# Performance work log

Measured on AMD Instinct MI355X. Metric: run time of the kernel, lower is better.

## Reference

```python
import jax, jax.numpy as jnp
import numpy as np
from jax import lax

N = 1024          # n_ligand == n_receptor == feature dim (required by broadcast in source)
D = 1024          # gnn_input_dim == gnn_output_dim
H = 32            # hopi_output_dim
C = 32            # cnn_channels


def setup_inputs() -> dict:
    key = jax.random.key(0)
    ks = jax.random.split(key, 24)
    s = 0.02
    inp = {
        "ligand_node_features": jax.random.normal(ks[0], (N, D), jnp.float32),
        "ligand_edge_features": jax.random.normal(ks[1], (N, D), jnp.float32),
        "ligand_adjacency": jax.random.uniform(ks[2], (N, N), jnp.float32),
        "receptor_node_features": jax.random.normal(ks[3], (N, D), jnp.float32),
        "receptor_edge_features": jax.random.normal(ks[4], (N, D), jnp.float32),
        "receptor_adjacency": jax.random.uniform(ks[5], (N, N), jnp.float32),
        # GNNLayer params (shared between ligand and receptor, as in source)
        "Wn": jax.random.normal(ks[6], (D, D), jnp.float32) * s,
        "bn": jax.random.normal(ks[7], (D,), jnp.float32) * s,
        "We": jax.random.normal(ks[8], (D, D), jnp.float32) * s,
        "be": jax.random.normal(ks[9], (D,), jnp.float32) * s,
        "Wa": jax.random.normal(ks[10], (1, D), jnp.float32) * s,
        "ba": jax.random.normal(ks[11], (1,), jnp.float32) * s,
        # HighOrderPairwiseInteraction: Linear(2*D -> H)
        "W_hopi": jax.random.normal(ks[12], (H, 2 * D), jnp.float32) * s,
        "b_hopi": jax.random.normal(ks[13], (H,), jnp.float32) * s,
        # CNN tail
        "conv1_w": jax.random.normal(ks[14], (C, H, 3, 3), jnp.float32) * s,
        "conv1_b": jax.random.normal(ks[15], (C,), jnp.float32) * s,
        "conv2_w": jax.random.normal(ks[16], (C, C, 3, 3), jnp.float32) * s,
        "conv2_b": jax.random.normal(ks[17], (C,), jnp.float32) * s,
        "conv3_w": jax.random.normal(ks[18], (1, C, 1, 1), jnp.float32) * s,
        "conv3_b": jax.random.normal(ks[19], (1,), jnp.float32) * s,
    }
    return inp


def _gnn(nf, ef, Wn, bn, We, be, Wa, ba):
    # aggregated: [N, D]
    agg = jnp.tanh(nf @ Wn.T + bn + ef @ We.T + be)
    scores = agg @ Wa.T + ba                      # [N, 1]
    attn = jax.nn.softmax(scores, axis=1)         # softmax over size-1 dim -> ones (faithful)
    weighted = jnp.sum(agg * attn, axis=1)        # [N]
    return nf + weighted                          # [N,D] + [N] broadcasts over last dim (D == N)


def _conv(x, w, b):
    y = lax.conv_general_dilated(x, w, (1, 1), "SAME",
                                 dimension_numbers=("NCHW", "OIHW", "NCHW"))
    return y + b[None, :, None, None]


def reference(ligand_node_features, ligand_edge_features, ligand_adjacency,
              receptor_node_features, receptor_edge_features, receptor_adjacency,
              Wn, bn, We, be, Wa, ba, W_hopi, b_hopi,
              conv1_w, conv1_b, conv2_w, conv2_b, conv3_w, conv3_b):
    lig = _gnn(ligand_node_features, ligand_edge_features, Wn, bn, We, be, Wa, ba)
    rec = _gnn(receptor_node_features, receptor_edge_features, Wn, bn, We, be, Wa, ba)

    # HOPI: interactions[i, j] = Linear(cat(lig[i], rec[j])) == lig[i] @ Wl.T + rec[j] @ Wr.T + b
    Wl, Wr = W_hopi[:, :D], W_hopi[:, D:]
    lig_p = lig @ Wl.T                            # [N, H]
    rec_p = rec @ Wr.T                            # [N, H]
    interactions = lig_p[:, None, :] + rec_p[None, :, :] + b_hopi  # [N, N, H]

    x = jnp.transpose(interactions, (2, 0, 1))[None]  # [1, H, N, N]
    x = jax.nn.relu(_conv(x, conv1_w, conv1_b))
    x = jax.nn.relu(_conv(x, conv2_w, conv2_b))
    x = _conv(x, conv3_w, conv3_b)                # [1, 1, N, N]
    return x[0, 0]                                # [N, N]
```

## Files before the change

### kernel.cpp

```cpp
#include <hip/hip_runtime.h>


typedef _Float16 half8 __attribute__((ext_vector_type(8)));
typedef _Float16 half4 __attribute__((ext_vector_type(4)));
typedef float    f32x4 __attribute__((ext_vector_type(4)));

__device__ __forceinline__ short f2h_bits(float f){
    _Float16 h = (_Float16)f;
    return __builtin_bit_cast(short, h);
}
__device__ __forceinline__ half8 pack2(const float4& x, const float4& y){
    half8 r;
    r[0] = (_Float16)x.x; r[1] = (_Float16)x.y;
    r[2] = (_Float16)x.z; r[3] = (_Float16)x.w;
    r[4] = (_Float16)y.x; r[5] = (_Float16)y.y;
    r[6] = (_Float16)y.z; r[7] = (_Float16)y.w;
    return r;
}
__device__ __forceinline__ float tanh_fast(float x){
    float e = __expf(2.f * x);
    return 1.f - 2.f / (e + 1.f);
}

#define SWZ(c) ((((c) >> 1) & 3) << 3)

__global__ __launch_bounds__(512) void gnn_kernel(
    const float* __restrict__ lig_nf, const float* __restrict__ lig_ef,
    const float* __restrict__ rec_nf, const float* __restrict__ rec_ef,
    const float* __restrict__ Wn, const float* __restrict__ We,
    const float* __restrict__ bn, const float* __restrict__ be,
    float* __restrict__ part)
{
    __shared__ __attribute__((aligned(16))) short As[128 * 64];
    __shared__ __attribute__((aligned(16))) short Bs[64 * 64];
    __shared__ float red[128][2];

    const int t  = threadIdx.x;
    const int cx = blockIdx.z;
    const float* A0 = cx ? rec_nf : lig_nf;
    const float* A1 = cx ? rec_ef : lig_ef;
    const int j0 = blockIdx.x * 128;
    const int d0 = blockIdx.y * 64;

    const int wid  = t >> 6;
    const int wm   = wid >> 1;
    const int wn   = wid & 1;
    const int lane = t & 63;
    const int lr   = lane & 15;
    const int lg   = lane >> 4;

    f32x4 acc[2][2];
    #pragma unroll
    for (int m = 0; m < 2; ++m)
        #pragma unroll
        for (int n = 0; n < 2; ++n)
            acc[m][n] = (f32x4){0.f, 0.f, 0.f, 0.f};

    const int arow = t >> 2;
    const int akc  = (t & 3) * 16;
    const int brow = t >> 3;
    const int bkc  = (t & 7) * 8;

    float4 av[4], bv[2];
    {
        const float* ap = A0 + (size_t)(j0 + arow) * 1024 + akc;
        const float* bp = Wn + (size_t)(d0 + brow) * 1024 + bkc;
        #pragma unroll
        for (int q = 0; q < 4; ++q) av[q] = *reinterpret_cast<const float4*>(ap + q * 4);
        #pragma unroll
        for (int q = 0; q < 2; ++q) bv[q] = *reinterpret_cast<const float4*>(bp + q * 4);
    }

    for (int kb = 0; kb < 2048; kb += 64){
        __syncthreads();
        {
            const int ga = (t & 3) * 2;
            const int sa = arow & 7;
            *reinterpret_cast<half8*>(&As[arow * 64 + ((ga    ) ^ sa) * 8]) = pack2(av[0], av[1]);
            *reinterpret_cast<half8*>(&As[arow * 64 + ((ga + 1) ^ sa) * 8]) = pack2(av[2], av[3]);
            *reinterpret_cast<half8*>(&Bs[brow * 64 + (((t & 7)) ^ (brow & 7)) * 8]) = pack2(bv[0], bv[1]);
        }
        {
            const int kbn = (kb + 64) & 2047;
            const float* Asrc = (kbn < 1024) ? A0 : A1;
            const float* Bsrc = (kbn < 1024) ? Wn : We;
            const int kk = kbn & 1023;
            const float* ap = Asrc + (size_t)(j0 + arow) * 1024 + kk + akc;
            const float* bp = Bsrc + (size_t)(d0 + brow) * 1024 + kk + bkc;
            #pragma unroll
            for (int q = 0; q < 4; ++q) av[q] = *reinterpret_cast<const float4*>(ap + q * 4);
            #pragma unroll
            for (int q = 0; q < 2; ++q) bv[q] = *reinterpret_cast<const float4*>(bp + q * 4);
        }
        __syncthreads();

        #pragma unroll
        for (int ks = 0; ks < 2; ++ks){
            half8 Af[2], Bf[2];
            #pragma unroll
            for (int m = 0; m < 2; ++m){
                int row = wm * 32 + m * 16 + lr;
                int g   = ((ks * 4 + lg) ^ (row & 7)) * 8;
                Af[m] = *reinterpret_cast<const half8*>(&As[row * 64 + g]);
            }
            #pragma unroll
            for (int n = 0; n < 2; ++n){
                int col = wn * 32 + n * 16 + lr;
                int g   = ((ks * 4 + lg) ^ (col & 7)) * 8;
                Bf[n] = *reinterpret_cast<const half8*>(&Bs[col * 64 + g]);
            }
            #pragma unroll
            for (int m = 0; m < 2; ++m)
                #pragma unroll
                for (int n = 0; n < 2; ++n)
                    acc[m][n] = __builtin_amdgcn_mfma_f32_16x16x32_f16(
                        Af[m], Bf[n], acc[m][n], 0, 0, 0);
        }
    }

    float rowsum[2][4];
    #pragma unroll
    for (int m = 0; m < 2; ++m)
        #pragma unroll
        for (int jj = 0; jj < 4; ++jj) rowsum[m][jj] = 0.f;
    #pragma unroll
    for (int n = 0; n < 2; ++n){
        int d = d0 + wn * 32 + n * 16 + lr;
        float bias = bn[d] + be[d];
        #pragma unroll
        for (int m = 0; m < 2; ++m)
            #pragma unroll
            for (int jj = 0; jj < 4; ++jj)
                rowsum[m][jj] += tanh_fast(acc[m][n][jj] + bias);
    }
    #pragma unroll
    for (int mask = 1; mask < 16; mask <<= 1)
        #pragma unroll
        for (int m = 0; m < 2; ++m)
            #pragma unroll
            for (int jj = 0; jj < 4; ++jj)
                rowsum[m][jj] += __shfl_xor(rowsum[m][jj], mask);
    __syncthreads();
    if (lr == 0){
        #pragma unroll
        for (int m = 0; m < 2; ++m)
            #pragma unroll
            for (int jj = 0; jj < 4; ++jj)
                red[wm * 32 + m * 16 + lg * 4 + jj][wn] = rowsum[m][jj];
    }
    __syncthreads();
    if (t < 128)
        part[(size_t)cx * 16384 + (size_t)blockIdx.y * 1024 + j0 + t]
            = red[t][0] + red[t][1];
}

__global__ __launch_bounds__(256) void pp_kernel(
    const float* __restrict__ lig_nf, const float* __restrict__ rec_nf,
    const float* __restrict__ W_hopi, const float* __restrict__ b_hopi,
    const float* __restrict__ w1, const float* __restrict__ b1,
    const float* __restrict__ w2,
    const float* __restrict__ part,
    float* __restrict__ Kp, short* __restrict__ U16, short* __restrict__ V16,
    short* __restrict__ w2f16)
{
    __shared__ __attribute__((aligned(16))) char smem[46208];
    const int t = threadIdx.x;
    const int role = blockIdx.x;

    if (role < 32){
        short* As = reinterpret_cast<short*>(smem);
        short* Bs = reinterpret_cast<short*>(smem + 10240);
        short* Pz = reinterpret_cast<short*>(smem + 14336);
        short* Ws = reinterpret_cast<short*>(smem + 20736);

        const int cx = role >> 4;
        const int r0 = (role & 15) * 64;
        const float* nf = cx ? rec_nf : lig_nf;
        const float* W  = W_hopi + (cx ? 1024 : 0);
        short* O = cx ? V16 : U16;

        const int wid = t >> 6;
        const int lane = t & 63;
        const int lr = lane & 15;
        const int lg = lane >> 4;

        for (int e = t; e < 9216; e += 256){
            int cs  = e / 3072;
            int rem = e - cs * 3072;
            int co  = rem / 96;
            int k   = rem - co * 96;
            int d   = k >> 5;
            int ci  = k & 31;
            int o_lo = (cs == 1) ? 1 : 0;
            int o_hi = (cs == 2) ? 1 : 2;
            float s = 0.f;
            for (int o = o_lo; o <= o_hi; ++o){
                int tap = cx ? (o * 3 + d) : (d * 3 + o);
                s += w1[co * 288 + ci * 9 + tap];
            }
            Ws[(cs * 32 + co) * 104 + k] = f2h_bits(s);
        }

        f32x4 acc[2][2];
        #pragma unroll
        for (int mi = 0; mi < 2; ++mi)
            #pragma unroll
            for (int n = 0; n < 2; ++n)
                acc[mi][n] = (f32x4){0.f, 0.f, 0.f, 0.f};

        for (int kb = 0; kb < 16; ++kb){
            const int kcol = kb * 64;
            __syncthreads();
            for (int e = t; e < 320; e += 256){
                int rowl = e >> 2;
                int grow = r0 - 8 + rowl;
                int chunk = (e & 3) * 16;
                float4 a0, a1, a2, a3;
                if ((unsigned)grow < 1024u){
                    const float* ap = nf + (size_t)grow * 1024 + kcol + chunk;
                    a0 = *reinterpret_cast<const float4*>(ap);
                    a1 = *reinterpret_cast<const float4*>(ap + 4);
                    a2 = *reinterpret_cast<const float4*>(ap + 8);
                    a3 = *reinterpret_cast<const float4*>(ap + 12);
                } else {
                    a0 = a1 = a2 = a3 = make_float4(0.f, 0.f, 0.f, 0.f);
                }
                int ga = (e & 3) * 2;
                int sa = rowl & 7;
                *reinterpret_cast<half8*>(&As[rowl * 64 + ((ga    ) ^ sa) * 8]) = pack2(a0, a1);
                *reinterpret_cast<half8*>(&As[rowl * 64 + ((ga + 1) ^ sa) * 8]) = pack2(a2, a3);
            }
            {
                int row = t >> 3;
                int kc  = (t & 7) * 8;
                const float* bp = W + (size_t)row * 2048 + kcol + kc;
                float4 b0 = *reinterpret_cast<const float4*>(bp);
                float4 b1 = *reinterpret_cast<const float4*>(bp + 4);
                *reinterpret_cast<half8*>(&Bs[row * 64 + ((t & 7) ^ (row & 7)) * 8]) = pack2(b0, b1);
            }
            __syncthreads();
            #pragma unroll
            for (int mi = 0; mi < 2; ++mi){
                int mf = wid + mi * 4;
                if (mf >= 5) break;
                #pragma unroll
                for (int ks = 0; ks < 2; ++ks){
                    int ar = mf * 16 + lr;
                    half8 Af = *reinterpret_cast<const half8*>(
                        &As[ar * 64 + ((ks * 4 + lg) ^ (ar & 7)) * 8]);
                    #pragma unroll
                    for (int n = 0; n < 2; ++n){
                        int col = n * 16 + lr;
                        half8 Bf = *reinterpret_cast<const half8*>(
                            &Bs[col * 64 + ((ks * 4 + lg) ^ (col & 7)) * 8]);
                        acc[mi][n] = __builtin_amdgcn_mfma_f32_16x16x32_f16(
                            Af, Bf, acc[mi][n], 0, 0, 0);
                    }
                }
            }
        }
        #pragma unroll
        for (int mi = 0; mi < 2; ++mi){
            int mf = wid + mi * 4;
            if (mf >= 5) break;
            #pragma unroll
            for (int n = 0; n < 2; ++n)
                #pragma unroll
                for (int jj = 0; jj < 4; ++jj){
                    int rowl = mf * 16 + lg * 4 + jj;
                    Pz[rowl * 40 + n * 16 + lr] = f2h_bits(acc[mi][n][jj]);
                }
        }
        __syncthreads();

        f32x4 uacc[3][2];
        #pragma unroll
        for (int cs = 0; cs < 3; ++cs)
            #pragma unroll
            for (int n = 0; n < 2; ++n)
                uacc[cs][n] = (f32x4){0.f, 0.f, 0.f, 0.f};
        #pragma unroll
        for (int d = 0; d < 3; ++d){
            int ar = wid * 16 + lr;
            half8 Ap = *reinterpret_cast<const half8*>(
                &Pz[(7 + ar + d) * 40 + lg * 8]);
            #pragma unroll
            for (int cs = 0; cs < 3; ++cs)
                #pragma unroll
                for (int n = 0; n < 2; ++n){
                    half8 Bp = *reinterpret_cast<const half8*>(
                        &Ws[(cs * 32 + n * 16 + lr) * 104 + d * 32 + lg * 8]);
                    uacc[cs][n] = __builtin_amdgcn_mfma_f32_16x16x32_f16(
                        Ap, Bp, uacc[cs][n], 0, 0, 0);
                }
        }
        #pragma unroll
        for (int cs = 0; cs < 3; ++cs)
            #pragma unroll
            for (int n = 0; n < 2; ++n)
                #pragma unroll
                for (int jj = 0; jj < 4; ++jj){
                    int grow = r0 + wid * 16 + lg * 4 + jj;
                    O[((size_t)(cs << 10) + grow) * 32 + n * 16 + lr]
                        = f2h_bits(uacc[cs][n][jj]);
                }
        return;
    }

    if (role == 33){
        for (int e = t; e < 9216; e += 256){
            int co  = e / 288;
            int rem = e - co * 288;
            int ci  = rem / 9;
            int tap = rem - ci * 9;
            w2f16[(tap * 32 + co) * 32 + (ci ^ SWZ(co))] = f2h_bits(w2[e]);
        }
        return;
    }

    float* ws_l = reinterpret_cast<float*>(smem);
    float* ws_r = reinterpret_cast<float*>(smem + 4096);
    float* red  = reinterpret_cast<float*>(smem + 8192);
    float* cvs  = reinterpret_cast<float*>(smem + 9216);
    float* w1s  = reinterpret_cast<float*>(smem + 9344);

    #pragma unroll
    for (int q = 0; q < 9; ++q){
        int idx = (t + q * 256) * 4;
        *reinterpret_cast<float4*>(&w1s[idx]) =
            *reinterpret_cast<const float4*>(w1 + idx);
    }
    for (int j = t; j < 1024; j += 256){
        float sl = 0.f, sr = 0.f;
        #pragma unroll
        for (int b = 0; b < 16; ++b){
            sl += part[b * 1024 + j];
            sr += part[16384 + b * 1024 + j];
        }
        ws_l[j] = sl; ws_r[j] = sr;
    }
    __syncthreads();
    {
        const int h = t & 31;
        const int seg = t >> 5;
        const float* wl = W_hopi + (size_t)h * 2048 + seg * 128;
        const float* wr = wl + 1024;
        float s = 0.f;
        #pragma unroll 8
        for (int j = 0; j < 128; j += 4){
            float4 a = *reinterpret_cast<const float4*>(wl + j);
            float4 b = *reinterpret_cast<const float4*>(wr + j);
            const float* l = &ws_l[seg * 128 + j];
            const float* r = &ws_r[seg * 128 + j];
            s = fmaf(l[0], a.x, s); s = fmaf(l[1], a.y, s);
            s = fmaf(l[2], a.z, s); s = fmaf(l[3], a.w, s);
            s = fmaf(r[0], b.x, s); s = fmaf(r[1], b.y, s);
            s = fmaf(r[2], b.z, s); s = fmaf(r[3], b.w, s);
        }
        red[t] = s;
    }
    __syncthreads();
    if (t < 32){
        float tot = b_hopi[t];
        #pragma unroll
        for (int g = 0; g < 8; ++g) tot += red[g * 32 + t];
        cvs[t] = tot;
    }
    __syncthreads();
    for (int e = t; e < 288; e += 256){
        int co  = e & 31;
        int cse = e >> 5;
        int yc  = cse / 3, xc = cse - yc * 3;
        float sum = b1[co];
        for (int ci = 0; ci < 32; ++ci){
            const float* wp = &w1s[co * 288 + ci * 9];
            float t00 = wp[0], t01 = wp[1], t02 = wp[2];
            float t10 = wp[3], t11 = wp[4], t12 = wp[5];
            float t20 = wp[6], t21 = wp[7], t22 = wp[8];
            float r0, r1, r2;
            if (xc == 0){ r0 = t00+t01+t02; r1 = t10+t11+t12; r2 = t20+t21+t22; }
            else if (xc == 1){ r0 = t01+t02; r1 = t11+t12; r2 = t21+t22; }
            else { r0 = t00+t01; r1 = t10+t11; r2 = t20+t21; }
            float wsum = (yc == 0) ? (r0+r1+r2) : ((yc == 1) ? (r1+r2) : (r0+r1));
            sum = fmaf(cvs[ci], wsum, sum);
        }
        Kp[cse * 32 + co] = sum;
    }
}

__global__ __launch_bounds__(512) void conv_kernel(
    const short* __restrict__ U16, const short* __restrict__ V16,
    const float* __restrict__ Kp, const short* __restrict__ w2f16,
    const float* __restrict__ b2,
    const float* __restrict__ w3, const float* __restrict__ b3,
    float* __restrict__ outp)
{
    __shared__ __attribute__((aligned(16))) short ys[18 * 18 * 32];
    __shared__ __attribute__((aligned(16))) short wB[9 * 32 * 32];

    const int t    = threadIdx.x;
    const int oy0  = blockIdx.y * 16;
    const int ox0  = blockIdx.x * 16;
    const int wid  = t >> 6;
    const int lane = t & 63;
    const int lr   = lane & 15;
    const int lg   = lane >> 4;

    {
        const uint4* src = reinterpret_cast<const uint4*>(w2f16);
        uint4* dst = reinterpret_cast<uint4*>(wB);
        #pragma unroll
        for (int e = t; e < 1152; e += 512)
            dst[e] = src[e];
    }
    #pragma unroll
    for (int pass = 0; pass < 6; ++pass){
        int idx = t + pass * 512;
        if (idx < 2592){
            int po  = idx >> 3;
            int cp  = (idx & 7) * 4;
            int ryo = po / 18;
            int rxo = po - ryo * 18;
            int gy = oy0 - 1 + ryo, gx = ox0 - 1 + rxo;
            half4 h = {(_Float16)0.f, (_Float16)0.f, (_Float16)0.f, (_Float16)0.f};
            if ((unsigned)gy < 1024u && (unsigned)gx < 1024u){
                int yc = (gy == 0) ? 1 : ((gy == 1023) ? 2 : 0);
                int xc = (gx == 0) ? 1 : ((gx == 1023) ? 2 : 0);
                half4 u = *reinterpret_cast<const half4*>(
                    &U16[((size_t)(xc << 10) + gy) * 32 + cp]);
                half4 v = *reinterpret_cast<const half4*>(
                    &V16[((size_t)(yc << 10) + gx) * 32 + cp]);
                float4 k = *reinterpret_cast<const float4*>(&Kp[(yc * 3 + xc) * 32 + cp]);
                h[0] = (_Float16)fmaxf((float)u[0] + (float)v[0] + k.x, 0.f);
                h[1] = (_Float16)fmaxf((float)u[1] + (float)v[1] + k.y, 0.f);
                h[2] = (_Float16)fmaxf((float)u[2] + (float)v[2] + k.z, 0.f);
                h[3] = (_Float16)fmaxf((float)u[3] + (float)v[3] + k.w, 0.f);
            }
            *reinterpret_cast<half4*>(&ys[po * 32 + (cp ^ SWZ(rxo))]) = h;
        }
    }
    __syncthreads();

    {
        half8 Bf[2][9];
        float bias[2], w3v[2];
        #pragma unroll
        for (int n = 0; n < 2; ++n){
            int co = n * 16 + lr;
            bias[n] = b2[co];
            w3v[n]  = w3[co];
            #pragma unroll
            for (int tap = 0; tap < 9; ++tap)
                Bf[n][tap] = *reinterpret_cast<const half8*>(
                    &wB[(tap * 32 + co) * 32 + ((lg * 8) ^ SWZ(co))]);
        }
        const float b3v = b3[0];
        for (int s = wid; s < 16; s += 8){
            int p  = s * 16 + lr;
            int ry = p >> 4;
            int rx = p & 15;
            f32x4 acc0 = {0.f, 0.f, 0.f, 0.f};
            f32x4 acc1 = {0.f, 0.f, 0.f, 0.f};
            #pragma unroll
            for (int tap = 0; tap < 9; ++tap){
                const int dy = tap / 3, dx = tap - (tap / 3) * 3;
                int pix = (ry + dy) * 18 + rx + dx;
                half8 A = *reinterpret_cast<const half8*>(
                    &ys[pix * 32 + ((lg * 8) ^ SWZ(rx + dx))]);
                acc0 = __builtin_amdgcn_mfma_f32_16x16x32_f16(A, Bf[0][tap], acc0, 0, 0, 0);
                acc1 = __builtin_amdgcn_mfma_f32_16x16x32_f16(A, Bf[1][tap], acc1, 0, 0, 0);
            }
            float part[4];
            #pragma unroll
            for (int j = 0; j < 4; ++j)
                part[j] = w3v[0] * fmaxf(acc0[j] + bias[0], 0.f)
                        + w3v[1] * fmaxf(acc1[j] + bias[1], 0.f);
            #pragma unroll
            for (int m = 1; m < 16; m <<= 1)
                #pragma unroll
                for (int j = 0; j < 4; ++j)
                    part[j] += __shfl_xor(part[j], m);
            if (lr == 0){
                float4 o = make_float4(part[0] + b3v, part[1] + b3v,
                                       part[2] + b3v, part[3] + b3v);
                *reinterpret_cast<float4*>(outp + (size_t)(oy0 + s) * 1024 + ox0 + lg * 4) = o;
            }
        }
    }
}

extern "C" void kernel_launch(void* const* d_in, const int* in_sizes, int n_in,
                              void* d_out, int out_size, void* d_ws, size_t ws_size,
                              hipStream_t stream)
{
    const float* lig_nf = (const float*)d_in[0];
    const float* lig_ef = (const float*)d_in[1];
    const float* rec_nf = (const float*)d_in[3];
    const float* rec_ef = (const float*)d_in[4];
    const float* Wn     = (const float*)d_in[6];
    const float* bn     = (const float*)d_in[7];
    const float* We     = (const float*)d_in[8];
    const float* be     = (const float*)d_in[9];
    const float* W_hopi = (const float*)d_in[12];
    const float* b_hopi = (const float*)d_in[13];
    const float* w1     = (const float*)d_in[14];
    const float* b1     = (const float*)d_in[15];
    const float* w2     = (const float*)d_in[16];
    const float* b2     = (const float*)d_in[17];
    const float* w3     = (const float*)d_in[18];
    const float* b3     = (const float*)d_in[19];
    float* outp = (float*)d_out;

    float* part  = (float*)d_ws;
    float* Kp    = (float*)((char*)d_ws + 393216);
    short* U16   = (short*)((char*)d_ws + 394368);
    short* V16   = (short*)((char*)d_ws + 590976);
    short* w2f16 = (short*)((char*)d_ws + 787584);

    dim3 g1(8, 16, 2);
    gnn_kernel<<<g1, 512, 0, stream>>>(lig_nf, lig_ef, rec_nf, rec_ef,
                                       Wn, We, bn, be, part);
    pp_kernel<<<34, 256, 0, stream>>>(lig_nf, rec_nf, W_hopi, b_hopi,
                                      w1, b1, w2, part, Kp, U16, V16, w2f16);
    dim3 g3(64, 64);
    conv_kernel<<<g3, 512, 0, stream>>>(U16, V16, Kp, w2f16, b2, w3, b3, outp);
}
```

Baseline: 124.1 us.

## Double-buffer GNN GEMM register prefetch and add fast interior path for conv2 staging

Result: faster. 117.9 us (-5.0%).

```diff
diff --git a/kernel.cpp b/kernel.cpp
--- a/kernel.cpp
+++ b/kernel.cpp
@@ -23,6 +23,54 @@
 }
 
 #define SWZ(c) ((((c) >> 1) & 3) << 3)
+
+#define GNN_LOAD(AV, BV, KBN) {                                              \
+    const int kbn_ = (KBN) & 2047;                                           \
+    const float* Asrc_ = (kbn_ < 1024) ? A0 : A1;                            \
+    const float* Bsrc_ = (kbn_ < 1024) ? Wn : We;                            \
+    const int kk_ = kbn_ & 1023;                                             \
+    const float* ap_ = Asrc_ + (size_t)(j0 + arow) * 1024 + kk_ + akc;       \
+    const float* bp_ = Bsrc_ + (size_t)(d0 + brow) * 1024 + kk_ + bkc;       \
+    AV[0] = *reinterpret_cast<const float4*>(ap_);                           \
+    AV[1] = *reinterpret_cast<const float4*>(ap_ + 4);                       \
+    AV[2] = *reinterpret_cast<const float4*>(ap_ + 8);                       \
+    AV[3] = *reinterpret_cast<const float4*>(ap_ + 12);                      \
+    BV[0] = *reinterpret_cast<const float4*>(bp_);                           \
+    BV[1] = *reinterpret_cast<const float4*>(bp_ + 4);                       \
+}
+
+#define GNN_STAGE(AV, BV) {                                                  \
+    const int ga_ = (t & 3) * 2;                                             \
+    const int sa_ = arow & 7;                                                \
+    *reinterpret_cast<half8*>(&As[arow * 64 + ((ga_    ) ^ sa_) * 8]) = pack2(AV[0], AV[1]); \
+    *reinterpret_cast<half8*>(&As[arow * 64 + ((ga_ + 1) ^ sa_) * 8]) = pack2(AV[2], AV[3]); \
+    *reinterpret_cast<half8*>(&Bs[brow * 64 + ((t & 7) ^ (brow & 7)) * 8]) = pack2(BV[0], BV[1]); \
+}
+
+#define GNN_MFMA() {                                                         \
+    _Pragma("unroll")                                                        \
+    for (int ks = 0; ks < 2; ++ks){                                          \
+        half8 Af[2], Bf[2];                                                  \
+        _Pragma("unroll")                                                    \
+        for (int m = 0; m < 2; ++m){                                         \
+            int row = wm * 32 + m * 16 + lr;                                 \
+            int g   = ((ks * 4 + lg) ^ (row & 7)) * 8;                       \
+            Af[m] = *reinterpret_cast<const half8*>(&As[row * 64 + g]);      \
+        }                                                                    \
+        _Pragma("unroll")                                                    \
+        for (int n = 0; n < 2; ++n){                                         \
+            int col = wn * 32 + n * 16 + lr;                                 \
+            int g   = ((ks * 4 + lg) ^ (col & 7)) * 8;                       \
+            Bf[n] = *reinterpret_cast<const half8*>(&Bs[col * 64 + g]);      \
+        }                                                                    \
+        _Pragma("unroll")                                                    \
+        for (int m = 0; m < 2; ++m)                                          \
+            _Pragma("unroll")                                                \
+            for (int n = 0; n < 2; ++n)                                      \
+                acc[m][n] = __builtin_amdgcn_mfma_f32_16x16x32_f16(          \
+                    Af[m], Bf[n], acc[m][n], 0, 0, 0);                       \
+    }                                                                        \
+}
 
 __global__ __launch_bounds__(512) void gnn_kernel(
     const float* __restrict__ lig_nf, const float* __restrict__ lig_ef,
@@ -61,61 +109,21 @@
     const int brow = t >> 3;
     const int bkc  = (t & 7) * 8;
 
-    float4 av[4], bv[2];
-    {
-        const float* ap = A0 + (size_t)(j0 + arow) * 1024 + akc;
-        const float* bp = Wn + (size_t)(d0 + brow) * 1024 + bkc;
-        #pragma unroll
-        for (int q = 0; q < 4; ++q) av[q] = *reinterpret_cast<const float4*>(ap + q * 4);
-        #pragma unroll
-        for (int q = 0; q < 2; ++q) bv[q] = *reinterpret_cast<const float4*>(bp + q * 4);
-    }
-
-    for (int kb = 0; kb < 2048; kb += 64){
+    float4 avA[4], bvA[2], avB[4], bvB[2];
+    GNN_LOAD(avA, bvA, 0);
+    GNN_LOAD(avB, bvB, 64);
+
+    for (int kb = 0; kb < 2048; kb += 128){
         __syncthreads();
-        {
-            const int ga = (t & 3) * 2;
-            const int sa = arow & 7;
-            *reinterpret_cast<half8*>(&As[arow * 64 + ((ga    ) ^ sa) * 8]) = pack2(av[0], av[1]);
-            *reinterpret_cast<half8*>(&As[arow * 64 + ((ga + 1) ^ sa) * 8]) = pack2(av[2], av[3]);
-            *reinterpret_cast<half8*>(&Bs[brow * 64 + (((t & 7)) ^ (brow & 7)) * 8]) = pack2(bv[0], bv[1]);
-        }
-        {
-            const int kbn = (kb + 64) & 2047;
-            const float* Asrc = (kbn < 1024) ? A0 : A1;
-            const float* Bsrc = (kbn < 1024) ? Wn : We;
-            const int kk = kbn & 1023;
-            const float* ap = Asrc + (size_t)(j0 + arow) * 1024 + kk + akc;
-            const float* bp = Bsrc + (size_t)(d0 + brow) * 1024 + kk + bkc;
-            #pragma unroll
-            for (int q = 0; q < 4; ++q) av[q] = *reinterpret_cast<const float4*>(ap + q * 4);
-            #pragma unroll
-            for (int q = 0; q < 2; ++q) bv[q] = *reinterpret_cast<const float4*>(bp + q * 4);
-        }
+        GNN_STAGE(avA, bvA);
+        GNN_LOAD(avA, bvA, kb + 128);
         __syncthreads();
-
-        #pragma unroll
-        for (int ks = 0; ks < 2; ++ks){
-            half8 Af[2], Bf[2];
-            #pragma unroll
-            for (int m = 0; m < 2; ++m){
-                int row = wm * 32 + m * 16 + lr;
-                int g   = ((ks * 4 + lg) ^ (row & 7)) * 8;
-                Af[m] = *reinterpret_cast<const half8*>(&As[row * 64 + g]);
-            }
-            #pragma unroll
-            for (int n = 0; n < 2; ++n){
-                int col = wn * 32 + n * 16 + lr;
-                int g   = ((ks * 4 + lg) ^ (col & 7)) * 8;
-                Bf[n] = *reinterpret_cast<const half8*>(&Bs[col * 64 + g]);
-            }
-            #pragma unroll
-            for (int m = 0; m < 2; ++m)
-                #pragma unroll
-                for (int n = 0; n < 2; ++n)
-                    acc[m][n] = __builtin_amdgcn_mfma_f32_16x16x32_f16(
-                        Af[m], Bf[n], acc[m][n], 0, 0, 0);
-        }
+        GNN_MFMA();
+        __syncthreads();
+        GNN_STAGE(avB, bvB);
+        GNN_LOAD(avB, bvB, kb + 192);
+        __syncthreads();
+        GNN_MFMA();
     }
 
     float rowsum[2][4];
@@ -413,30 +421,59 @@
         for (int e = t; e < 1152; e += 512)
             dst[e] = src[e];
     }
-    #pragma unroll
-    for (int pass = 0; pass < 6; ++pass){
-        int idx = t + pass * 512;
-        if (idx < 2592){
-            int po  = idx >> 3;
-            int cp  = (idx & 7) * 4;
-            int ryo = po / 18;
-            int rxo = po - ryo * 18;
-            int gy = oy0 - 1 + ryo, gx = ox0 - 1 + rxo;
-            half4 h = {(_Float16)0.f, (_Float16)0.f, (_Float16)0.f, (_Float16)0.f};
-            if ((unsigned)gy < 1024u && (unsigned)gx < 1024u){
-                int yc = (gy == 0) ? 1 : ((gy == 1023) ? 2 : 0);
-                int xc = (gx == 0) ? 1 : ((gx == 1023) ? 2 : 0);
-                half4 u = *reinterpret_cast<const half4*>(
-                    &U16[((size_t)(xc << 10) + gy) * 32 + cp]);
-                half4 v = *reinterpret_cast<const half4*>(
-                    &V16[((size_t)(yc << 10) + gx) * 32 + cp]);
-                float4 k = *reinterpret_cast<const float4*>(&Kp[(yc * 3 + xc) * 32 + cp]);
-                h[0] = (_Float16)fmaxf((float)u[0] + (float)v[0] + k.x, 0.f);
-                h[1] = (_Float16)fmaxf((float)u[1] + (float)v[1] + k.y, 0.f);
-                h[2] = (_Float16)fmaxf((float)u[2] + (float)v[2] + k.z, 0.f);
-                h[3] = (_Float16)fmaxf((float)u[3] + (float)v[3] + k.w, 0.f);
-            }
-            *reinterpret_cast<half4*>(&ys[po * 32 + (cp ^ SWZ(rxo))]) = h;
+    const bool interior = (blockIdx.x >= 1) & (blockIdx.x <= 62) &
+                          (blockIdx.y >= 1) & (blockIdx.y <= 62);
+    if (interior){
+        const int cp = (t & 7) * 4;
+        half4 k00;
+        {
+            float4 kf = *reinterpret_cast<const float4*>(&Kp[cp]);
+            k00[0] = (_Float16)kf.x; k00[1] = (_Float16)kf.y;
+            k00[2] = (_Float16)kf.z; k00[3] = (_Float16)kf.w;
+        }
+        #pragma unroll
+        for (int pass = 0; pass < 6; ++pass){
+            int idx = t + pass * 512;
+            if (idx < 2592){
+                int po  = idx >> 3;
+                int ryo = po / 18;
+                int rxo = po - ryo * 18;
+                int gy = oy0 - 1 + ryo, gx = ox0 - 1 + rxo;
+                half4 u = *reinterpret_cast<const half4*>(&U16[gy * 32 + cp]);
+                half4 v = *reinterpret_cast<const half4*>(&V16[gx * 32 + cp]);
+                half4 r = u + v + k00;
+                #pragma unroll
+                for (int e = 0; e < 4; ++e)
+                    r[e] = r[e] > (_Float16)0.f ? r[e] : (_Float16)0.f;
+                *reinterpret_cast<half4*>(&ys[po * 32 + (cp ^ SWZ(rxo))]) = r;
+            }
+        }
+    } else {
+        #pragma unroll
+        for (int pass = 0; pass < 6; ++pass){
+            int idx = t + pass * 512;
+            if (idx < 2592){
+                int po  = idx >> 3;
+                int cp  = (idx & 7) * 4;
+                int ryo = po / 18;
+                int rxo = po - ryo * 18;
+                int gy = oy0 - 1 + ryo, gx = ox0 - 1 + rxo;
+                half4 h = {(_Float16)0.f, (_Float16)0.f, (_Float16)0.f, (_Float16)0.f};
+                if ((unsigned)gy < 1024u && (unsigned)gx < 1024u){
+                    int yc = (gy == 0) ? 1 : ((gy == 1023) ? 2 : 0);
+                    int xc = (gx == 0) ? 1 : ((gx == 1023) ? 2 : 0);
+                    half4 u = *reinterpret_cast<const half4*>(
+                        &U16[((size_t)(xc << 10) + gy) * 32 + cp]);
+                    half4 v = *reinterpret_cast<const half4*>(
+                        &V16[((size_t)(yc << 10) + gx) * 32 + cp]);
+                    float4 k = *reinterpret_cast<const float4*>(&Kp[(yc * 3 + xc) * 32 + cp]);
+                    h[0] = (_Float16)fmaxf((float)u[0] + (float)v[0] + k.x, 0.f);
+                    h[1] = (_Float16)fmaxf((float)u[1] + (float)v[1] + k.y, 0.f);
+                    h[2] = (_Float16)fmaxf((float)u[2] + (float)v[2] + k.z, 0.f);
+                    h[3] = (_Float16)fmaxf((float)u[3] + (float)v[3] + k.w, 0.f);
+                }
+                *reinterpret_cast<half4*>(&ys[po * 32 + (cp ^ SWZ(rxo))]) = h;
+            }
         }
     }
     __syncthreads();
```
